# Optimization experiments

Hardware: AMD Instinct MI355X
Metric: run time of the kernel (lower is better)

## Reference

```python
import jax, jax.numpy as jnp
import numpy as np

# eval_para constants (init_kwargs)
RM = 100.0          # r_max
RN = 1000           # r_dsc (radial grid points)
L_MAX = 2
PARA1 = 1.0
RD = RM / RN        # radial step
MR = int(RN * 0.1)  # matching radius index = 100
E_BATCH = 4096

R = jnp.linspace(RM / RN, RM, RN, dtype=jnp.float32).reshape(RN, 1, 1)      # r grid
L = jnp.arange(L_MAX + 1, dtype=jnp.float32).reshape(1, 1, -1)               # l values
FACT = jnp.asarray([np.prod([2 * li + 1 for li in range(lm + 1)])
                    for lm in range(L_MAX + 1)], dtype=jnp.float32)          # (2l+1)!! = [1,3,15]


def disc_solve(sol_init, factor):
    """4th-order Numerov-style recurrence, faithful to the torch loop
    (including the original operator precedence: the 1/(1 - 3/40 rd^2 f[i+4])
    divisor applies only to the sol[i] term)."""
    rd2 = RD * RD
    a = 2.0 + (13.0 / 15.0) * rd2 * factor
    b = -2.0 + (7.0 / 60.0) * rd2 * factor
    c = -1.0 + (3.0 / 40.0) * rd2 * factor
    d = 1.0 - (3.0 / 40.0) * rd2 * factor
    xs = (a[3:RN - 1], b[2:RN - 2], a[1:RN - 3], c[:RN - 4], d[4:])  # each [RN-4, E, L]

    def step(carry, x):
        s0, s1, s2, s3 = carry
        a3, b2, a1, c0, d4 = x
        new = s3 * a3 + s2 * b2 + s1 * a1 + s0 * c0 / d4
        return (s1, s2, s3, new), new

    init = (sol_init[0], sol_init[1], sol_init[2], sol_init[3])
    _, ys = jax.lax.scan(step, init, xs)
    return jnp.concatenate([sol_init[:4], ys], axis=0)


def derivative(f, at):
    # 4th-order backward finite difference
    return (25.0 * f[at] - 48.0 * f[at - 1] + 36.0 * f[at - 2]
            - 16.0 * f[at - 3] + 3.0 * f[at - 4]) / (12.0 * RD)


def integrate_sq(f, n):
    """Faithful port of EvalEig.integrate: n panels of width 4*RD starting at
    index 0 (the original ignores the start offset and leaves f[4i+2] unsquared)."""
    f0 = f[0:4 * n:4]
    f1 = f[1:4 * n + 1:4]
    f2 = f[2:4 * n + 2:4]
    f3 = f[3:4 * n + 3:4]
    f4 = f[4:4 * n + 4:4]
    return ((7.0 * (f0 ** 2 + f4 ** 2) + 32.0 * (f1 ** 2 + f3 ** 2)
             + 12.0 * f2) * (2.0 * RD / 45.0)).sum(0)


def _forward(init_energy):
    E = init_energy.shape[0]
    energy = jnp.broadcast_to(init_energy[:, None], (E, L_MAX + 1))  # [E, L]

    # diffeq_factor with coulomb potential -1/r
    e = energy[None]                                    # [1, E, L]
    factor = L * (L + 1.0) / R ** 2 + PARA1 * (-e - 1.0 / R)  # [RN, E, L]

    # u_zero series initial condition near r=0
    u0_init = jnp.broadcast_to(
        R ** (L + 1.0) + R ** (L + 2.0) / (2.0 * (L + 1.0)) * (-PARA1),
        factor.shape)

    # u_infty initial condition: r * spherical-bessel-like series
    x = R * jnp.sqrt(jnp.abs(e))                        # [RN, E, L]
    base = x ** L / FACT
    h = x * x / 2.0
    series = 1.0 + h / (2.0 * L + 3.0) + h * h / (2.0 * (2.0 * L + 3.0) * (2.0 * L + 5.0))
    ui_init = R * base * series

    # dual propagation: outward and (flipped) inward Numerov scans
    u_zero = disc_solve(u0_init, factor)
    u_infty = jnp.flip(disc_solve(ui_init, jnp.flip(factor, 0)), 0)

    # matching: log-derivative mismatch / norm -> Newton energy step
    lf_in = derivative(u_zero, MR) / u_zero[MR]
    lf_out = derivative(u_infty, MR) / u_infty[MR]
    integ_in = integrate_sq(u_zero, MR // 4 - 1)
    integ_out = integrate_sq(u_infty, (RN - MR) // 4 - 1)
    delta = -(lf_out - lf_in) / (integ_in / u_zero[MR] ** 2 + integ_out / u_infty[MR] ** 2)
    return energy + delta


def setup_inputs() -> dict:
    key = jax.random.key(0)
    init_energy = jax.random.uniform(key, (E_BATCH,), dtype=jnp.float32)
    return {"init_energy": init_energy}


def reference(init_energy) -> jnp.ndarray:
    return _forward(init_energy)
```

## Files before the change

### kernel.cpp

```cpp
#include <hip/hip_runtime.h>
#include <math.h>

#pragma clang fp contract(off)


__device__ __forceinline__ float fmul32(float a, float b) { return a * b; }
__device__ __forceinline__ float fadd32(float a, float b) { return a + b; }
__device__ __forceinline__ float fsub32(float a, float b) { return a - b; }
#define FMA32(a, b, c) __builtin_fmaf((a), (b), (c))

__global__ __launch_bounds__(64)
void eval_eig_kernel(const float* __restrict__ ein, float* __restrict__ out, int ntot) {
  constexpr double RD64  = 100.0 / 1000.0;
  constexpr double RD2   = RD64 * RD64;
  constexpr float  KA32  = (float)(13.0 / 15.0 * RD2);
  constexpr float  KB32  = (float)( 7.0 / 60.0 * RD2);
  constexpr float  KC32  = (float)( 3.0 / 40.0 * RD2);
  constexpr float  nKC32 = -KC32;
  constexpr float  DRD32 = (float)(12.0 * RD64);
  constexpr float  ISC32 = (float)(2.0 * RD64 / 45.0);
  constexpr double Q64   = (100.0 - 0.1) / 999.0;

  __shared__ __align__(16) float2 tv[3][1000];
  __shared__ float gbuf[224][64];

  for (int t = threadIdx.x; t < 3000; t += 64) {
    int li = t / 1000, i = t - li * 1000;
    double y = (double)i * Q64 + 0.1;
    float r  = (i == 999) ? 100.0f : (float)y;
    float r2 = fmul32(r, r);
    float num = (float)(li * (li + 1));
    tv[li][i] = make_float2(num / r2, 1.0f / r);
  }
  __syncthreads();

  const int tid = blockIdx.x * 64 + threadIdx.x;
  if (tid >= ntot) return;
  const int b = tid / 3;
  const int l = tid - b * 3;
  const float e  = ein[b];
  const float me = -e;
  const float2* __restrict__ tvl = tv[l];

  struct Coef { float a, bc, d, y2; };
  auto MKC = [&](float tx, float ty) -> Coef {
    Coef c;
    float f  = fadd32(tx, fsub32(me, ty));
    c.a  = FMA32(KA32, f, 2.0f);
    c.bc = FMA32(KB32, f, -2.0f);
    c.d  = FMA32(nKC32, f, 1.0f);
    float y0 = __builtin_amdgcn_rcpf(c.d);
    float e0 = FMA32(-c.d, y0, 1.0f);
    float y1 = FMA32(y0, e0, y0);
    float e1 = FMA32(-c.d, y1, 1.0f);
    c.y2 = FMA32(y1, e1, y1);
    return c;
  };

  float s0, s1, s2, s3;
  float a_m1, a_m2, a_m3, b_m1, b_m2, d_m1, d_m2, d_m3, d_m4;
  auto CSTEP = [&](const Coef& c) {
    float n  = fmul32(s0, d_m4);
    float q0 = fmul32(n, c.y2);
    float r  = FMA32(-c.d, q0, n);
    float w  = FMA32(r, c.y2, q0);
    float m2 = fmul32(s2, b_m2);
    float t1 = FMA32(s3, a_m1, m2);
    float t2 = FMA32(s1, a_m3, -w);
    float u  = fadd32(t1, t2);
    d_m4 = d_m3; d_m3 = d_m2; d_m2 = d_m1; d_m1 = c.d;
    a_m3 = a_m2; a_m2 = a_m1; a_m1 = c.a;
    b_m2 = b_m1; b_m1 = c.bc;
    s0 = s1; s1 = s2; s2 = s3; s3 = u;
  };

  auto FVAL = [&](int idx) -> float {
    float2 t_ = tvl[idx];
    return fadd32(t_.x, fsub32(me, t_.y));
  };
  auto SEED = [&](float f0, float f1, float f2v, float f3) {
    a_m1 = FMA32(KA32, f3, 2.0f);
    a_m2 = FMA32(KA32, f2v, 2.0f);
    a_m3 = FMA32(KA32, f1, 2.0f);
    b_m1 = FMA32(KB32, f3, -2.0f);
    b_m2 = FMA32(KB32, f2v, -2.0f);
    d_m1 = FMA32(nKC32, f3, 1.0f);
    d_m2 = FMA32(nKC32, f2v, 1.0f);
    d_m3 = FMA32(nKC32, f1, 1.0f);
    d_m4 = FMA32(nKC32, f0, 1.0f);
  };
  auto PANEL = [&](float f0, float f1, float f2v, float f3, float f4) -> float {
    float s1q = FMA32(f0, f0, fmul32(f4, f4));
    float s3q = FMA32(f1, f1, fmul32(f3, f3));
    float t   = FMA32(7.0f, s1q, fmul32(32.0f, s3q));
    float g   = FMA32(12.0f, f2v, t);
    return fmul32(g, ISC32);
  };
  auto DER5 = [&](float f4, float f3, float f2v, float f1, float f0) -> float {
    float m48 = fmul32(48.0f, f3);
    float d1  = FMA32(25.0f, f4, -m48);
    float d2  = FMA32(36.0f, f2v, d1);
    float d3  = FMA32(-16.0f, f1, d2);
    float d4v = FMA32(3.0f, f0, d3);
    return d4v / DRD32;
  };

  float rr[4];
  #pragma unroll
  for (int i = 0; i < 4; ++i) rr[i] = (float)((double)i * Q64 + 0.1);

  float lf_in, lf_out, integ_in, integ_out, u100v, v899;

  {
    #pragma unroll
    for (int i = 0; i < 4; ++i) {
      double rd = (double)rr[i];
      double r2 = rd * rd;
      float p1, p2;
      if (l == 0)      { p1 = rr[i];            p2 = (float)r2;        }
      else if (l == 1) { p1 = (float)r2;        p2 = (float)(r2 * rd); }
      else             { p1 = (float)(r2 * rd); p2 = (float)(r2 * r2); }
      float q  = p2 / (float)(2 * (l + 1));
      float u0 = fsub32(p1, q);
      if (i == 0) s0 = u0; else if (i == 1) s1 = u0; else if (i == 2) s2 = u0; else s3 = u0;
    }
    SEED(FVAL(0), FVAL(1), FVAL(2), FVAL(3));

    float p0 = s0, p1 = s1, p2 = s2, p3 = s3;
    { float2 t4 = tvl[4]; Coef c = MKC(t4.x, t4.y); CSTEP(c); }
    float accI = PANEL(p0, p1, p2, p3, s3);
    float pb = s3;
    #pragma unroll 2
    for (int k = 1; k < 24; ++k) {
      int base = 4 * k;
      float2 t1v = tvl[base + 1], t2v = tvl[base + 2];
      float2 t3v = tvl[base + 3], t4v = tvl[base + 4];
      Coef c1 = MKC(t1v.x, t1v.y), c2 = MKC(t2v.x, t2v.y);
      Coef c3 = MKC(t3v.x, t3v.y), c4 = MKC(t4v.x, t4v.y);
      CSTEP(c1); float q1 = s3;
      CSTEP(c2); float q2 = s3;
      CSTEP(c3); float q3 = s3;
      CSTEP(c4); float q4 = s3;
      accI = fadd32(accI, PANEL(pb, q1, q2, q3, q4));
      pb = q4;
    }
    float u96 = pb;
    float2 t97 = tvl[97], t98 = tvl[98], t99 = tvl[99], t100 = tvl[100];
    Coef c97 = MKC(t97.x, t97.y), c98 = MKC(t98.x, t98.y);
    Coef c99 = MKC(t99.x, t99.y), c100 = MKC(t100.x, t100.y);
    CSTEP(c97);  float u97 = s3;
    CSTEP(c98);  float u98 = s3;
    CSTEP(c99);  float u99 = s3;
    CSTEP(c100); u100v = s3;
    integ_in = accI;
    lf_in = DER5(u100v, u99, u98, u97, u96) / u100v;
  }

  {
    float sq = (float)sqrt((double)fabsf(e));
    #pragma unroll
    for (int i = 0; i < 4; ++i) {
      float x    = fmul32(rr[i], sq);
      float xl   = (l == 0) ? 1.0f : ((l == 1) ? x : fmul32(x, x));
      float fact = (l == 0) ? 1.0f : ((l == 1) ? 3.0f : 15.0f);
      float base = xl / fact;
      float h  = fmul32(x, x) / 2.0f;
      float c1 = (float)(2 * l + 3);
      float c2 = (float)(2 * (2 * l + 3) * (2 * l + 5));
      float t2 = fadd32(1.0f, h / c1);
      float series = fadd32(t2, fmul32(h, h) / c2);
      float ui = fmul32(fmul32(rr[i], base), series);
      if (i == 0) s0 = ui; else if (i == 1) s1 = ui; else if (i == 2) s2 = ui; else s3 = ui;
    }
    SEED(FVAL(999), FVAL(998), FVAL(997), FVAL(996));

    float4 lo = *(const float4*)&tvl[992];
    float4 hi = *(const float4*)&tvl[994];
    #pragma unroll 2
    for (int g = 0; g < 25; ++g) {
      Coef c3 = MKC(hi.z, hi.w), c2 = MKC(hi.x, hi.y);
      Coef c1 = MKC(lo.z, lo.w), c0 = MKC(lo.x, lo.y);
      if (g < 24) {
        int m0 = 992 - 4 * (g + 1);
        lo = *(const float4*)&tvl[m0];
        hi = *(const float4*)&tvl[m0 + 2];
      }
      CSTEP(c3); CSTEP(c2); CSTEP(c1); CSTEP(c0);
    }
    float r4v = s3;

    float v900, v901, v902, v903;
    lo = *(const float4*)&tvl[4 * 223];
    hi = *(const float4*)&tvl[4 * 223 + 2];
    #define BGROUP(P)                                                          \
      Coef c3 = MKC(hi.z, hi.w), c2 = MKC(hi.x, hi.y);                         \
      Coef c1 = MKC(lo.z, lo.w), c0 = MKC(lo.x, lo.y);                         \
      if ((P) > 0) {                                                           \
        lo = *(const float4*)&tvl[4 * (P) - 4];                                \
        hi = *(const float4*)&tvl[4 * (P) - 2];                                \
      }                                                                        \
      CSTEP(c3); float f3v = s3;                                               \
      CSTEP(c2); float f2w = s3;                                               \
      CSTEP(c1); float f1v = s3;                                               \
      CSTEP(c0); float f0v = s3;                                               \
      gbuf[(P)][threadIdx.x] = PANEL(f0v, f1v, f2w, f3v, r4v);                 \
      r4v = f0v;

    #pragma unroll 2
    for (int p = 223; p >= 26; --p) { BGROUP(p); }
    { BGROUP(25); v899 = f0v; }
    { BGROUP(24); v900 = f3v; v901 = f2w; v902 = f1v; v903 = f0v; }
    #pragma unroll 2
    for (int p = 23; p >= 0; --p) { BGROUP(p); }
    #undef BGROUP

    float accO = gbuf[0][threadIdx.x];
    for (int p = 1; p < 224; ++p) accO = fadd32(accO, gbuf[p][threadIdx.x]);
    integ_out = accO;
    lf_out = DER5(v899, v900, v901, v902, v903) / v899;
  }

  float uzsq = fmul32(u100v, u100v);
  float uisq = fmul32(v899, v899);
  float den  = fadd32(integ_in / uzsq, integ_out / uisq);
  float dnum = fsub32(lf_out, lf_in);
  float delta = (-dnum) / den;
  out[tid] = fadd32(e, delta);
}

extern "C" void kernel_launch(void* const* d_in, const int* in_sizes, int n_in,
                              void* d_out, int out_size, void* d_ws, size_t ws_size,
                              hipStream_t stream) {
  const float* ein = (const float*)d_in[0];
  float* out = (float*)d_out;
  int ntot = in_sizes[0] * 3;
  int grid = (ntot + 63) / 64;
  eval_eig_kernel<<<dim3(grid), dim3(64), 0, stream>>>(ein, out, ntot);
}
```

Before: 62.74 us.

## Batch recurrence steps in groups of four and accumulate outward integral in registers

Adds a four-step combined update that computes all four divided terms from the old state before chaining the dependent additions. This moves the reciprocal-correction work off the serial critical path of the Numerov recurrence. It also drops the shared-memory panel buffer and sums the outward integral in a register, in reverse panel order, which changes float rounding slightly. Launch bounds now request one block per CU, and removing the large shared buffer frees LDS.

```diff
diff --git a/kernel.cpp b/kernel.cpp
--- a/kernel.cpp
+++ b/kernel.cpp
@@ -9,7 +9,9 @@
 __device__ __forceinline__ float fsub32(float a, float b) { return a - b; }
 #define FMA32(a, b, c) __builtin_fmaf((a), (b), (c))
 
-__global__ __launch_bounds__(64)
+struct Coef { float a, bc, d, y2; };
+
+__global__ __launch_bounds__(64, 1)
 void eval_eig_kernel(const float* __restrict__ ein, float* __restrict__ out, int ntot) {
   constexpr double RD64  = 100.0 / 1000.0;
   constexpr double RD2   = RD64 * RD64;
@@ -22,7 +24,6 @@
   constexpr double Q64   = (100.0 - 0.1) / 999.0;
 
   __shared__ __align__(16) float2 tv[3][1000];
-  __shared__ float gbuf[224][64];
 
   for (int t = threadIdx.x; t < 3000; t += 64) {
     int li = t / 1000, i = t - li * 1000;
@@ -42,7 +43,11 @@
   const float me = -e;
   const float2* __restrict__ tvl = tv[l];
 
-  struct Coef { float a, bc, d, y2; };
+  float s0, s1, s2, s3;
+  float cd1, cd2, cd3, cd4;
+  float ca1, ca2, ca3;
+  float cb1, cb2;
+
   auto MKC = [&](float tx, float ty) -> Coef {
     Coef c;
     float f  = fadd32(tx, fsub32(me, ty));
@@ -56,22 +61,50 @@
     c.y2 = FMA32(y1, e1, y1);
     return c;
   };
-
-  float s0, s1, s2, s3;
-  float a_m1, a_m2, a_m3, b_m1, b_m2, d_m1, d_m2, d_m3, d_m4;
-  auto CSTEP = [&](const Coef& c) {
-    float n  = fmul32(s0, d_m4);
+  auto WC = [&](float sv, float dold, const Coef& c) -> float {
+    float n  = fmul32(sv, dold);
     float q0 = fmul32(n, c.y2);
     float r  = FMA32(-c.d, q0, n);
-    float w  = FMA32(r, c.y2, q0);
-    float m2 = fmul32(s2, b_m2);
-    float t1 = FMA32(s3, a_m1, m2);
-    float t2 = FMA32(s1, a_m3, -w);
+    return FMA32(r, c.y2, q0);
+  };
+  auto SSTEP = [&](const Coef& c) {
+    float w  = WC(s0, cd4, c);
+    float m2 = fmul32(s2, cb2);
+    float t1 = FMA32(s3, ca1, m2);
+    float t2 = FMA32(s1, ca3, -w);
     float u  = fadd32(t1, t2);
-    d_m4 = d_m3; d_m3 = d_m2; d_m2 = d_m1; d_m1 = c.d;
-    a_m3 = a_m2; a_m2 = a_m1; a_m1 = c.a;
-    b_m2 = b_m1; b_m1 = c.bc;
+    cd4 = cd3; cd3 = cd2; cd2 = cd1; cd1 = c.d;
+    ca3 = ca2; ca2 = ca1; ca1 = c.a;
+    cb2 = cb1; cb1 = c.bc;
     s0 = s1; s1 = s2; s2 = s3; s3 = u;
+  };
+  auto G4 = [&](const Coef& e1c, const Coef& e2c, const Coef& e3c, const Coef& e4c,
+                float& uo1, float& uo2, float& uo3, float& uo4) {
+    float w1 = WC(s0, cd4, e1c);
+    float w2 = WC(s1, cd3, e2c);
+    float w3 = WC(s2, cd2, e3c);
+    float w4 = WC(s3, cd1, e4c);
+    float m1 = fmul32(s2, cb2);
+    float t11 = FMA32(s3, ca1, m1);
+    float t21 = FMA32(s1, ca3, -w1);
+    float u1 = fadd32(t11, t21);
+    float m2 = fmul32(s3, cb1);
+    float t22 = FMA32(s2, ca2, -w2);
+    float t12 = FMA32(u1, e1c.a, m2);
+    float u2 = fadd32(t12, t22);
+    float m3 = fmul32(u1, e1c.bc);
+    float t23 = FMA32(s3, ca1, -w3);
+    float t13 = FMA32(u2, e2c.a, m3);
+    float u3 = fadd32(t13, t23);
+    float m4 = fmul32(u2, e2c.bc);
+    float t24 = FMA32(u1, e1c.a, -w4);
+    float t14 = FMA32(u3, e3c.a, m4);
+    float u4 = fadd32(t14, t24);
+    cd4 = e1c.d; cd3 = e2c.d; cd2 = e3c.d; cd1 = e4c.d;
+    ca3 = e2c.a; ca2 = e3c.a; ca1 = e4c.a;
+    cb2 = e3c.bc; cb1 = e4c.bc;
+    s0 = u1; s1 = u2; s2 = u3; s3 = u4;
+    uo1 = u1; uo2 = u2; uo3 = u3; uo4 = u4;
   };
 
   auto FVAL = [&](int idx) -> float {
@@ -79,15 +112,15 @@
     return fadd32(t_.x, fsub32(me, t_.y));
   };
   auto SEED = [&](float f0, float f1, float f2v, float f3) {
-    a_m1 = FMA32(KA32, f3, 2.0f);
-    a_m2 = FMA32(KA32, f2v, 2.0f);
-    a_m3 = FMA32(KA32, f1, 2.0f);
-    b_m1 = FMA32(KB32, f3, -2.0f);
-    b_m2 = FMA32(KB32, f2v, -2.0f);
-    d_m1 = FMA32(nKC32, f3, 1.0f);
-    d_m2 = FMA32(nKC32, f2v, 1.0f);
-    d_m3 = FMA32(nKC32, f1, 1.0f);
-    d_m4 = FMA32(nKC32, f0, 1.0f);
+    ca1 = FMA32(KA32, f3, 2.0f);
+    ca2 = FMA32(KA32, f2v, 2.0f);
+    ca3 = FMA32(KA32, f1, 2.0f);
+    cb1 = FMA32(KB32, f3, -2.0f);
+    cb2 = FMA32(KB32, f2v, -2.0f);
+    cd1 = FMA32(nKC32, f3, 1.0f);
+    cd2 = FMA32(nKC32, f2v, 1.0f);
+    cd3 = FMA32(nKC32, f1, 1.0f);
+    cd4 = FMA32(nKC32, f0, 1.0f);
   };
   auto PANEL = [&](float f0, float f1, float f2v, float f3, float f4) -> float {
     float s1q = FMA32(f0, f0, fmul32(f4, f4));
@@ -127,7 +160,7 @@
     SEED(FVAL(0), FVAL(1), FVAL(2), FVAL(3));
 
     float p0 = s0, p1 = s1, p2 = s2, p3 = s3;
-    { float2 t4 = tvl[4]; Coef c = MKC(t4.x, t4.y); CSTEP(c); }
+    { float2 t4 = tvl[4]; SSTEP(MKC(t4.x, t4.y)); }
     float accI = PANEL(p0, p1, p2, p3, s3);
     float pb = s3;
     #pragma unroll 2
@@ -137,10 +170,8 @@
       float2 t3v = tvl[base + 3], t4v = tvl[base + 4];
       Coef c1 = MKC(t1v.x, t1v.y), c2 = MKC(t2v.x, t2v.y);
       Coef c3 = MKC(t3v.x, t3v.y), c4 = MKC(t4v.x, t4v.y);
-      CSTEP(c1); float q1 = s3;
-      CSTEP(c2); float q2 = s3;
-      CSTEP(c3); float q3 = s3;
-      CSTEP(c4); float q4 = s3;
+      float q1, q2, q3, q4;
+      G4(c1, c2, c3, c4, q1, q2, q3, q4);
       accI = fadd32(accI, PANEL(pb, q1, q2, q3, q4));
       pb = q4;
     }
@@ -148,10 +179,11 @@
     float2 t97 = tvl[97], t98 = tvl[98], t99 = tvl[99], t100 = tvl[100];
     Coef c97 = MKC(t97.x, t97.y), c98 = MKC(t98.x, t98.y);
     Coef c99 = MKC(t99.x, t99.y), c100 = MKC(t100.x, t100.y);
-    CSTEP(c97);  float u97 = s3;
-    CSTEP(c98);  float u98 = s3;
-    CSTEP(c99);  float u99 = s3;
-    CSTEP(c100); u100v = s3;
+    float u97, u98, u99;
+    SSTEP(c97);  u97 = s3;
+    SSTEP(c98);  u98 = s3;
+    SSTEP(c99);  u99 = s3;
+    SSTEP(c100); u100v = s3;
     integ_in = accI;
     lf_in = DER5(u100v, u99, u98, u97, u96) / u100v;
   }
@@ -178,32 +210,32 @@
     float4 hi = *(const float4*)&tvl[994];
     #pragma unroll 2
     for (int g = 0; g < 25; ++g) {
-      Coef c3 = MKC(hi.z, hi.w), c2 = MKC(hi.x, hi.y);
-      Coef c1 = MKC(lo.z, lo.w), c0 = MKC(lo.x, lo.y);
+      Coef e1c = MKC(hi.z, hi.w), e2c = MKC(hi.x, hi.y);
+      Coef e3c = MKC(lo.z, lo.w), e4c = MKC(lo.x, lo.y);
       if (g < 24) {
         int m0 = 992 - 4 * (g + 1);
         lo = *(const float4*)&tvl[m0];
         hi = *(const float4*)&tvl[m0 + 2];
       }
-      CSTEP(c3); CSTEP(c2); CSTEP(c1); CSTEP(c0);
+      float x1, x2, x3, x4;
+      G4(e1c, e2c, e3c, e4c, x1, x2, x3, x4);
     }
     float r4v = s3;
+    float accO = 0.0f;
 
     float v900, v901, v902, v903;
     lo = *(const float4*)&tvl[4 * 223];
     hi = *(const float4*)&tvl[4 * 223 + 2];
     #define BGROUP(P)                                                          \
-      Coef c3 = MKC(hi.z, hi.w), c2 = MKC(hi.x, hi.y);                         \
-      Coef c1 = MKC(lo.z, lo.w), c0 = MKC(lo.x, lo.y);                         \
+      Coef e1c = MKC(hi.z, hi.w), e2c = MKC(hi.x, hi.y);                       \
+      Coef e3c = MKC(lo.z, lo.w), e4c = MKC(lo.x, lo.y);                       \
       if ((P) > 0) {                                                           \
         lo = *(const float4*)&tvl[4 * (P) - 4];                                \
         hi = *(const float4*)&tvl[4 * (P) - 2];                                \
       }                                                                        \
-      CSTEP(c3); float f3v = s3;                                               \
-      CSTEP(c2); float f2w = s3;                                               \
-      CSTEP(c1); float f1v = s3;                                               \
-      CSTEP(c0); float f0v = s3;                                               \
-      gbuf[(P)][threadIdx.x] = PANEL(f0v, f1v, f2w, f3v, r4v);                 \
+      float f3v, f2w, f1v, f0v;                                                \
+      G4(e1c, e2c, e3c, e4c, f3v, f2w, f1v, f0v);                              \
+      accO = fadd32(accO, PANEL(f0v, f1v, f2w, f3v, r4v));                     \
       r4v = f0v;
 
     #pragma unroll 2
@@ -214,8 +246,6 @@
     for (int p = 23; p >= 0; --p) { BGROUP(p); }
     #undef BGROUP
 
-    float accO = gbuf[0][threadIdx.x];
-    for (int p = 1; p < 224; ++p) accO = fadd32(accO, gbuf[p][threadIdx.x]);
     integ_out = accO;
     lf_out = DER5(v899, v900, v901, v902, v903) / v899;
   }
```

New measurement: 60.23 us (median of 2 runs). -4.0%, faster.
